# Kernel tuning notes

Measured on AMD Instinct MI355X. Metric: run time of the kernel, lower is better.

The kernel has to match this reference:

```python
import jax, jax.numpy as jnp
import numpy as np

N, D, H, B, E = 100000, 256, 256, 128, 128
STEPS = 5


def setup_inputs() -> dict:
    key = jax.random.key(0)
    ks = jax.random.split(key, 16)
    w = lambda i, shape: (jax.random.normal(ks[i], shape, jnp.float32) * 0.05)
    inp = {
        "x": jax.random.normal(ks[0], (N, D), jnp.float32),
        "batch_idxs": jnp.sort(jax.random.randint(ks[1], (N,), 0, B)),
        # FNN: Linear(D,H) -> ELU -> Linear(H,H)
        "fnn_W1": w(2, (D, H)), "fnn_b1": jnp.zeros((H,), jnp.float32),
        "fnn_W2": w(3, (H, H)), "fnn_b2": jnp.zeros((H,), jnp.float32),
        # 3-layer LSTM, input 2H (layer 0) / H (layers 1,2), hidden H
        "Wih0": w(4, (4 * H, 2 * H)), "Whh0": w(5, (4 * H, H)),
        "bih0": jnp.zeros((4 * H,), jnp.float32), "bhh0": jnp.zeros((4 * H,), jnp.float32),
        "Wih1": w(6, (4 * H, H)), "Whh1": w(7, (4 * H, H)),
        "bih1": jnp.zeros((4 * H,), jnp.float32), "bhh1": jnp.zeros((4 * H,), jnp.float32),
        "Wih2": w(8, (4 * H, H)), "Whh2": w(9, (4 * H, H)),
        "bih2": jnp.zeros((4 * H,), jnp.float32), "bhh2": jnp.zeros((4 * H,), jnp.float32),
        # output Linear(2H, E)
        "out_W": w(10, (2 * H, E)), "out_b": jnp.zeros((E,), jnp.float32),
    }
    return inp


def _lstm_cell(xin, h, c, Wih, Whh, bih, bhh):
    gates = xin @ Wih.T + bih + h @ Whh.T + bhh  # (B, 4H)
    i, f, g, o = jnp.split(gates, 4, axis=-1)    # PyTorch gate order i,f,g,o
    c = jax.nn.sigmoid(f) * c + jax.nn.sigmoid(i) * jnp.tanh(g)
    h = jax.nn.sigmoid(o) * jnp.tanh(c)
    return h, c


def reference(x, batch_idxs, fnn_W1, fnn_b1, fnn_W2, fnn_b2,
              Wih0, Whh0, bih0, bhh0, Wih1, Whh1, bih1, bhh1,
              Wih2, Whh2, bih2, bhh2, out_W, out_b):
    # FNN (ELU between layers)
    hfeat = jax.nn.elu(x @ fnn_W1 + fnn_b1) @ fnn_W2 + fnn_b2  # (N, H)

    Wihs, Whhs = (Wih0, Wih1, Wih2), (Whh0, Whh1, Whh2)
    bihs, bhhs = (bih0, bih1, bih2), (bhh0, bhh1, bhh2)
    hs = [jnp.zeros((B, H), hfeat.dtype) for _ in range(3)]
    cs = [jnp.zeros((B, H), hfeat.dtype) for _ in range(3)]
    q_star = jnp.zeros((B, 2 * H), hfeat.dtype)

    for _ in range(STEPS):
        layer_in = q_star
        for l in range(3):
            hs[l], cs[l] = _lstm_cell(layer_in, hs[l], cs[l], Wihs[l], Whhs[l], bihs[l], bhhs[l])
            layer_in = hs[l]
        q = layer_in  # (B, H)
        # segment (per-graph) attention softmax over nodes
        e = jnp.sum(hfeat * q[batch_idxs], axis=-1)                     # (N,)
        m = jax.ops.segment_max(e, batch_idxs, num_segments=B)
        m = jnp.where(jnp.isfinite(m), m, 0.0)                          # guard empty segments
        ex = jnp.exp(e - m[batch_idxs])
        denom = jax.ops.segment_sum(ex, batch_idxs, num_segments=B) + 1e-16
        a = ex / denom[batch_idxs]                                      # (N,)
        r = jax.ops.segment_sum(a[:, None] * hfeat, batch_idxs, num_segments=B)  # (B, H)
        q_star = jnp.concatenate([q, r], axis=-1)                       # (B, 2H)

    return q_star @ out_W + out_b  # (B, E)
```

## Files before the change

### kernel.cpp

```cpp
#include <hip/hip_runtime.h>

#define NN 100000
#define NSTEP 5
#define LSTR 264

typedef unsigned short ushort_t;
typedef __attribute__((ext_vector_type(8))) short short8;
typedef __attribute__((ext_vector_type(4))) float floatx4;

__device__ __forceinline__ ushort_t f2bf(float f){
  union { float f; unsigned u; } v; v.f = f;
  unsigned r = v.u + 0x7fffu + ((v.u >> 16) & 1u);
  return (ushort_t)(r >> 16);
}
__device__ __forceinline__ float bf2f(ushort_t s){
  union { unsigned u; float f; } v; v.u = ((unsigned)s) << 16;
  return v.f;
}
__device__ __forceinline__ float sigf(float x){ return 1.0f/(1.0f+__expf(-x)); }

__global__ __launch_bounds__(512, 4) void fnn_fused(const float* __restrict__ x,
    const ushort_t* __restrict__ W1P, const float* __restrict__ b1,
    const ushort_t* __restrict__ W2P, const float* __restrict__ b2,
    ushort_t* __restrict__ hfeat, int M)
{
  __shared__ ushort_t buf[64 * LSTR];
  int tid = threadIdx.x;
  int w = tid >> 6, lane = tid & 63, qd = lane >> 4, r16 = lane & 15;
  int row0 = blockIdx.x * 64;
  int col0 = w * 32;

  {
    float4 xv[8];
    #pragma unroll
    for (int it = 0; it < 8; it++){
      int idx = it * 512 + tid;
      int rg = row0 + (idx >> 6); if (rg >= M) rg = M - 1;
      xv[it] = *(const float4*)(x + (size_t)rg * 256 + (idx & 63) * 4);
    }
    #pragma unroll
    for (int it = 0; it < 8; it++){
      int idx = it * 512 + tid;
      ushort4 pk = make_ushort4(f2bf(xv[it].x), f2bf(xv[it].y), f2bf(xv[it].z), f2bf(xv[it].w));
      *(ushort4*)&buf[(idx >> 6) * LSTR + (idx & 63) * 4] = pk;
    }
  }
  __syncthreads();

  floatx4 acc[4][2];

  #pragma unroll
  for (int i=0;i<4;i++)
    #pragma unroll
    for (int j=0;j<2;j++) acc[i][j] = (floatx4){0.f,0.f,0.f,0.f};

  #pragma unroll
  for (int kc = 0; kc < 8; kc++){
    short8 af[4], bfr[2];
    #pragma unroll
    for (int i=0;i<4;i++)
      af[i] = *(const short8*)&buf[(i*16 + r16) * LSTR + kc*32 + qd*8];
    #pragma unroll
    for (int j=0;j<2;j++)
      bfr[j] = *(const short8*)(W1P + (size_t)(((w*2 + j)*8 + kc)*64 + lane)*8);
    #pragma unroll
    for (int i=0;i<4;i++)
      #pragma unroll
      for (int j=0;j<2;j++)
        acc[i][j] = __builtin_amdgcn_mfma_f32_16x16x32_bf16(af[i], bfr[j], acc[i][j], 0, 0, 0);
  }
  __syncthreads();

  #pragma unroll
  for (int i=0;i<4;i++){
    #pragma unroll
    for (int j=0;j<2;j++){
      int col = col0 + j*16 + r16;
      float bb = b1[col];
      #pragma unroll
      for (int rr=0;rr<4;rr++){
        int row = i*16 + qd*4 + rr;
        float v = acc[i][j][rr] + bb;
        v = v > 0.f ? v : (__expf(v) - 1.0f);
        buf[row * LSTR + col] = f2bf(v);
      }
    }
  }
  __syncthreads();

  #pragma unroll
  for (int i=0;i<4;i++)
    #pragma unroll
    for (int j=0;j<2;j++) acc[i][j] = (floatx4){0.f,0.f,0.f,0.f};

  #pragma unroll
  for (int kc = 0; kc < 8; kc++){
    short8 af[4], bfr[2];
    #pragma unroll
    for (int i=0;i<4;i++)
      af[i] = *(const short8*)&buf[(i*16 + r16) * LSTR + kc*32 + qd*8];
    #pragma unroll
    for (int j=0;j<2;j++)
      bfr[j] = *(const short8*)(W2P + (size_t)(((w*2 + j)*8 + kc)*64 + lane)*8);
    #pragma unroll
    for (int i=0;i<4;i++)
      #pragma unroll
      for (int j=0;j<2;j++)
        acc[i][j] = __builtin_amdgcn_mfma_f32_16x16x32_bf16(af[i], bfr[j], acc[i][j], 0, 0, 0);
  }

  #pragma unroll
  for (int i=0;i<4;i++){
    #pragma unroll
    for (int j=0;j<2;j++){
      int col = col0 + j*16 + r16;
      float bb = b2[col];
      #pragma unroll
      for (int rr=0;rr<4;rr++){
        int row = row0 + i*16 + qd*4 + rr;
        if (row < M) hfeat[(size_t)row * 256 + col] = f2bf(acc[i][j][rr] + bb);
      }
    }
  }
}

__global__ __launch_bounds__(256) void lstm_layer(const ushort_t* __restrict__ A, int lda,
    const ushort_t* __restrict__ WcP, const float* __restrict__ bcp, int KC,
    float* __restrict__ c, ushort_t* __restrict__ dstA, int sA,
    ushort_t* __restrict__ dstB, int sB, float* __restrict__ qdst)
{
  __shared__ float sbuf[3][4][256];
  int tid = threadIdx.x, w = tid >> 6, lane = tid & 63, qd = lane >> 4, r16 = lane & 15;
  int m0 = (blockIdx.x & 7) * 16, nt = blockIdx.x >> 3;
  int kcq = KC >> 2;
  int kc0 = w * kcq;

  floatx4 acc[4];
  #pragma unroll
  for (int g=0; g<4; g++) acc[g] = (floatx4){0.f,0.f,0.f,0.f};

  const ushort_t* Ar = A + (size_t)(m0 + r16) * lda + qd * 8;
  for (int kc = kc0; kc < kc0 + kcq; kc++){
    short8 av = *(const short8*)(Ar + kc*32);
    #pragma unroll
    for (int g = 0; g < 4; g++){
      short8 bv = *(const short8*)(WcP + (size_t)((((g*16 + nt)*KC) + kc)*64 + lane)*8);
      acc[g] = __builtin_amdgcn_mfma_f32_16x16x32_bf16(av, bv, acc[g], 0, 0, 0);
    }
  }
  if (w){
    #pragma unroll
    for (int g=0; g<4; g++) *(floatx4*)&sbuf[w-1][g][lane*4] = acc[g];
  }
  __syncthreads();
  if (w == 0){
    #pragma unroll
    for (int g=0; g<4; g++)
      #pragma unroll
      for (int t=0; t<3; t++){
        floatx4 p = *(floatx4*)&sbuf[t][g][lane*4];
        acc[g] = acc[g] + p;
      }
    int h = nt*16 + r16;
    float bci = bcp[h], bcf = bcp[256+h], bcg = bcp[512+h], bco = bcp[768+h];
    #pragma unroll
    for (int rr=0; rr<4; rr++){
      int row = m0 + qd*4 + rr;
      float gi = acc[0][rr] + bci;
      float gf = acc[1][rr] + bcf;
      float gg = acc[2][rr] + bcg;
      float go = acc[3][rr] + bco;
      float cp = c[row*256 + h];
      float cn = sigf(gf)*cp + sigf(gi)*tanhf(gg);
      float hn = sigf(go)*tanhf(cn);
      c[row*256 + h] = cn;
      ushort_t hb = f2bf(hn);
      dstA[row*sA + h] = hb;
      dstB[row*sB + h] = hb;
      if (qdst) qdst[row*512 + h] = hn;
    }
  }
}

__global__ __launch_bounds__(256) void attn_onepass(const ushort_t* __restrict__ hfeat,
    const int* __restrict__ seg, const float* __restrict__ q_star,
    float* __restrict__ r_part, float* __restrict__ z_part)
{
  __shared__ float sred[4][260];
  int b = blockIdx.x >> 3, p = blockIdx.x & 7;
  int w = threadIdx.x >> 6, lane = threadIdx.x & 63;
  int s0 = seg[b], s1 = seg[b+1];
  int len = s1 - s0;
  int q0 = s0 + ((len * p) >> 3);
  int q1 = s0 + ((len * (p+1)) >> 3);

  float S0=0.f, S1=0.f, S2=0.f, S3=0.f, Z=0.f;

  int n = q0 + w;
  if (n < q1){
    float4 q = *(const float4*)(q_star + (size_t)b*512 + lane*4);
    #define LOADH(nn) (*(const ushort4*)(hfeat + (size_t)(nn)*256 + lane*4))
    ushort4 ha = LOADH(n);
    ushort4 hb = ha;
    if (n + 4 < q1) hb = LOADH(n + 4);
    for (; n < q1; n += 8){
      ushort4 hc = ha, hd = hb;
      if (n + 8  < q1) hc = LOADH(n + 8);
      if (n + 12 < q1) hd = LOADH(n + 12);
      float a0=bf2f(ha.x), a1=bf2f(ha.y), a2=bf2f(ha.z), a3=bf2f(ha.w);
      float da = a0*q.x + a1*q.y + a2*q.z + a3*q.w;
      float b0=0.f,b1=0.f,b2=0.f,b3=0.f, db=0.f;
      int vB = (n + 4) < q1;
      if (vB){
        b0=bf2f(hb.x); b1=bf2f(hb.y); b2=bf2f(hb.z); b3=bf2f(hb.w);
        db = b0*q.x + b1*q.y + b2*q.z + b3*q.w;
      }
      #pragma unroll
      for (int off = 32; off; off >>= 1){
        da += __shfl_xor(da, off);
        db += __shfl_xor(db, off);
      }
      float wa = __expf(da);
      Z += wa; S0 += wa*a0; S1 += wa*a1; S2 += wa*a2; S3 += wa*a3;
      if (vB){
        float wb = __expf(db);
        Z += wb; S0 += wb*b0; S1 += wb*b1; S2 += wb*b2; S3 += wb*b3;
      }
      ha = hc; hb = hd;
    }
    #undef LOADH
  }

  *(float4*)&sred[w][lane*4] = (float4){S0, S1, S2, S3};
  if (lane == 0) sred[w][256] = Z;
  __syncthreads();
  int f = threadIdx.x;
  if (f < 256){
    float v = sred[0][f] + sred[1][f] + sred[2][f] + sred[3][f];
    r_part[((size_t)p*128 + b)*256 + f] = v;
    if (f == 0)
      z_part[p*128 + b] = sred[0][256] + sred[1][256] + sred[2][256] + sred[3][256];
  }
}

__global__ __launch_bounds__(256) void attn_fin(const float* __restrict__ r_part,
    const float* __restrict__ z_part, float* __restrict__ q_star, ushort_t* __restrict__ xc0,
    const float* __restrict__ outW, const float* __restrict__ outb,
    float* __restrict__ out, int last)
{
  __shared__ float qs[512];
  int b = blockIdx.x, f = threadIdx.x;
  float s = 0.f, z = 0.f;
  #pragma unroll
  for (int t = 0; t < 8; t++){
    s += r_part[((size_t)(t*128 + b))*256 + f];
    z += z_part[t*128 + b];
  }
  float v = s / (z + 1e-16f);
  q_star[b*512 + 256 + f] = v;
  xc0[b*768 + 256 + f] = f2bf(v);
  if (last){
    qs[f] = q_star[b*512 + f];
    qs[256 + f] = v;
    __syncthreads();
    if (f < 128){
      float acc = outb[f];
      for (int k = 0; k < 512; k++) acc += qs[k] * outW[k*128 + f];
      out[b*128 + f] = acc;
    }
  }
}

__global__ void prep_all(const float* __restrict__ W1, const float* __restrict__ W2,
    const float* __restrict__ Wih0, const float* __restrict__ Whh0,
    const float* __restrict__ Wih1, const float* __restrict__ Whh1,
    const float* __restrict__ Wih2, const float* __restrict__ Whh2,
    const float* __restrict__ bih0, const float* __restrict__ bhh0,
    const float* __restrict__ bih1, const float* __restrict__ bhh1,
    const float* __restrict__ bih2, const float* __restrict__ bhh2,
    const int* __restrict__ bidx,
    ushort_t* __restrict__ W1P, ushort_t* __restrict__ W2P,
    ushort_t* __restrict__ Wc0P, ushort_t* __restrict__ Wc1P, ushort_t* __restrict__ Wc2P,
    float* __restrict__ c, ushort_t* __restrict__ xc, float* __restrict__ q_star,
    float* __restrict__ bc, int* __restrict__ seg)
{
  int i = blockIdx.x*256 + threadIdx.x;
  if (i < 131072){
    const float* W = (i < 65536) ? W1 : W2;
    ushort_t* P = (i < 65536) ? W1P : W2P;
    int r = i & 65535;
    int T = r >> 12, r2 = r & 4095;
    int kc = r2 >> 9, l = (r2 >> 3) & 63, j = r2 & 7;
    int k = kc*32 + ((l>>4)<<3) + j;
    int n = T*16 + (l & 15);
    P[r] = f2bf(W[k*256 + n]);
    return;
  }
  i -= 131072;
  if (i < 786432){
    int T = i / 12288, r2 = i - T*12288;
    int kc = r2 >> 9, l = (r2 >> 3) & 63, j = r2 & 7;
    int k = kc*32 + ((l>>4)<<3) + j;
    int g = T >> 4, n = (T & 15)*16 + (l & 15);
    int row = g*256 + n;
    Wc0P[i] = f2bf(k < 512 ? Wih0[row*512 + k] : Whh0[row*256 + (k - 512)]);
    return;
  }
  i -= 786432;
  if (i < 1048576){
    const float* Wih = (i < 524288) ? Wih1 : Wih2;
    const float* Whh = (i < 524288) ? Whh1 : Whh2;
    ushort_t* P = (i < 524288) ? Wc1P : Wc2P;
    int r = i & 524287;
    int T = r >> 13, r2 = r & 8191;
    int kc = r2 >> 9, l = (r2 >> 3) & 63, j = r2 & 7;
    int k = kc*32 + ((l>>4)<<3) + j;
    int g = T >> 4, n = (T & 15)*16 + (l & 15);
    int row = g*256 + n;
    P[r] = f2bf(k < 256 ? Wih[row*256 + k] : Whh[row*256 + (k - 256)]);
    return;
  }
  i -= 1048576;
  if (i < 98304) { c[i] = 0.f; return; }
  i -= 98304;
  if (i < 229376) { xc[i] = 0; return; }
  i -= 229376;
  if (i < 65536) { q_star[i] = 0.f; return; }
  i -= 65536;
  if (i < 3072) {
    int l = i >> 10, g = i & 1023;
    const float* bi = (l == 0) ? bih0 : ((l == 1) ? bih1 : bih2);
    const float* bh = (l == 0) ? bhh0 : ((l == 1) ? bhh1 : bhh2);
    bc[i] = bi[g] + bh[g];
    return;
  }
  i -= 3072;
  if (i < 129) {
    int lo = 0, hi = NN;
    while (lo < hi){ int mid = (lo + hi) >> 1; if (bidx[mid] < i) lo = mid + 1; else hi = mid; }
    seg[i] = lo;
    return;
  }
}

extern "C" void kernel_launch(void* const* d_in, const int* in_sizes, int n_in,
                              void* d_out, int out_size, void* d_ws, size_t ws_size,
                              hipStream_t stream)
{
  const float* x    = (const float*)d_in[0];
  const int*   bidx = (const int*)  d_in[1];
  const float* W1   = (const float*)d_in[2];
  const float* b1   = (const float*)d_in[3];
  const float* W2   = (const float*)d_in[4];
  const float* b2   = (const float*)d_in[5];
  const float* Wih0 = (const float*)d_in[6];
  const float* Whh0 = (const float*)d_in[7];
  const float* bih0 = (const float*)d_in[8];
  const float* bhh0 = (const float*)d_in[9];
  const float* Wih1 = (const float*)d_in[10];
  const float* Whh1 = (const float*)d_in[11];
  const float* bih1 = (const float*)d_in[12];
  const float* bhh1 = (const float*)d_in[13];
  const float* Wih2 = (const float*)d_in[14];
  const float* Whh2 = (const float*)d_in[15];
  const float* bih2 = (const float*)d_in[16];
  const float* bhh2 = (const float*)d_in[17];
  const float* outW = (const float*)d_in[18];
  const float* outb = (const float*)d_in[19];

  char* p = (char*)d_ws;
  auto alloc = [&](size_t bytes)->char*{ char* r = p; p += (bytes + 255) & ~(size_t)255; return r; };
  ushort_t* hfeat  = (ushort_t*)alloc((size_t)NN*256*2);
  ushort_t* W1P    = (ushort_t*)alloc(65536*2);
  ushort_t* W2P    = (ushort_t*)alloc(65536*2);
  ushort_t* Wc0P   = (ushort_t*)alloc(786432*2);
  ushort_t* Wc1P   = (ushort_t*)alloc(524288*2);
  ushort_t* Wc2P   = (ushort_t*)alloc(524288*2);
  float*    bc     = (float*)   alloc(3072*4);
  float*    c_all  = (float*)   alloc(98304*4);
  ushort_t* xc     = (ushort_t*)alloc(229376*2);
  float*    q_star = (float*)   alloc(65536*4);
  float*    r_part = (float*)   alloc(8*128*256*4);
  float*    z_part = (float*)   alloc(8*128*4);
  int*      seg    = (int*)     alloc(129*4);

  ushort_t* xc0 = xc;
  ushort_t* xc1 = xc + 98304;
  ushort_t* xc2 = xc + 163840;
  float* c0 = c_all, *c1 = c_all + 32768, *c2 = c_all + 65536;
  float* bc0 = bc, *bc1 = bc + 1024, *bc2 = bc + 2048;

  prep_all<<<9229, 256, 0, stream>>>(W1, W2, Wih0, Whh0, Wih1, Whh1, Wih2, Whh2,
                                     bih0, bhh0, bih1, bhh1, bih2, bhh2, bidx,
                                     W1P, W2P, Wc0P, Wc1P, Wc2P,
                                     c_all, xc, q_star, bc, seg);

  fnn_fused<<<1563, 512, 0, stream>>>(x, W1P, b1, W2P, b2, hfeat, NN);

  for (int s = 0; s < NSTEP; s++){
    lstm_layer<<<128, 256, 0, stream>>>(xc0, 768, Wc0P, bc0, 24, c0, xc0 + 512, 768, xc1, 512, nullptr);
    lstm_layer<<<128, 256, 0, stream>>>(xc1, 512, Wc1P, bc1, 16, c1, xc1 + 256, 512, xc2, 512, nullptr);
    lstm_layer<<<128, 256, 0, stream>>>(xc2, 512, Wc2P, bc2, 16, c2, xc2 + 256, 512, xc0, 768, q_star);
    attn_onepass<<<1024, 256, 0, stream>>>(hfeat, seg, q_star, r_part, z_part);
    attn_fin<<<128, 256, 0, stream>>>(r_part, z_part, q_star, xc0, outW, outb,
                                      (float*)d_out, s == NSTEP-1 ? 1 : 0);
  }
}
```

Baseline: 414.6 us.

## Fuse attention finalize into next LSTM layer, pipeline FNN loads, unroll attention

The per-step attn_fin reduction now happens inside the first LSTM layer of the next step, which reads the partial sums from a transposed r_part layout and stages the result in shared memory. This removes one kernel launch per step, and a single final kernel produces the output. The FNN GEMM loops are double-buffered so LDS and weight loads overlap the MFMAs, and the occupancy hint is dropped. The attention loop processes four nodes per wave per iteration with deeper prefetch. The LSTM kernel is templated on KC so its K loop can be fully unrolled, at the cost of redundant finalize work in each of the 16 column blocks that share a row group.

```diff
diff --git a/kernel.cpp b/kernel.cpp
--- a/kernel.cpp
+++ b/kernel.cpp
@@ -19,7 +19,7 @@
 }
 __device__ __forceinline__ float sigf(float x){ return 1.0f/(1.0f+__expf(-x)); }
 
-__global__ __launch_bounds__(512, 4) void fnn_fused(const float* __restrict__ x,
+__global__ __launch_bounds__(512) void fnn_fused(const float* __restrict__ x,
     const ushort_t* __restrict__ W1P, const float* __restrict__ b1,
     const ushort_t* __restrict__ W2P, const float* __restrict__ b2,
     ushort_t* __restrict__ hfeat, int M)
@@ -30,6 +30,25 @@
   int row0 = blockIdx.x * 64;
   int col0 = w * 32;
 
+  floatx4 acc[4][2];
+  short8 afA[4], afB[4], bfA[2], bfB[2];
+
+  auto LDA = [&](short8* d, int kc){
+    #pragma unroll
+    for (int i=0;i<4;i++) d[i] = *(const short8*)&buf[(i*16 + r16)*LSTR + kc*32 + qd*8];
+  };
+  auto LDW = [&](short8* d, const ushort_t* P, int kc){
+    #pragma unroll
+    for (int j=0;j<2;j++) d[j] = *(const short8*)(P + (size_t)(((w*2 + j)*8 + kc)*64 + lane)*8);
+  };
+  auto MM = [&](short8* a, short8* b){
+    #pragma unroll
+    for (int i=0;i<4;i++)
+      #pragma unroll
+      for (int j=0;j<2;j++)
+        acc[i][j] = __builtin_amdgcn_mfma_f32_16x16x32_bf16(a[i], b[j], acc[i][j], 0, 0, 0);
+  };
+
   {
     float4 xv[8];
     #pragma unroll
@@ -45,32 +64,24 @@
       *(ushort4*)&buf[(idx >> 6) * LSTR + (idx & 63) * 4] = pk;
     }
   }
-  __syncthreads();
-
-  floatx4 acc[4][2];
+  LDW(bfA, W1P, 0);
+  __syncthreads();
 
   #pragma unroll
   for (int i=0;i<4;i++)
     #pragma unroll
     for (int j=0;j<2;j++) acc[i][j] = (floatx4){0.f,0.f,0.f,0.f};
-
-  #pragma unroll
-  for (int kc = 0; kc < 8; kc++){
-    short8 af[4], bfr[2];
-    #pragma unroll
-    for (int i=0;i<4;i++)
-      af[i] = *(const short8*)&buf[(i*16 + r16) * LSTR + kc*32 + qd*8];
-    #pragma unroll
-    for (int j=0;j<2;j++)
-      bfr[j] = *(const short8*)(W1P + (size_t)(((w*2 + j)*8 + kc)*64 + lane)*8);
-    #pragma unroll
-    for (int i=0;i<4;i++)
-      #pragma unroll
-      for (int j=0;j<2;j++)
-        acc[i][j] = __builtin_amdgcn_mfma_f32_16x16x32_bf16(af[i], bfr[j], acc[i][j], 0, 0, 0);
-  }
-  __syncthreads();
-
+  LDA(afA, 0);
+  #pragma unroll
+  for (int kc = 0; kc < 8; kc += 2){
+    if (kc + 1 < 8){ LDA(afB, kc+1); LDW(bfB, W1P, kc+1); }
+    MM(afA, bfA);
+    if (kc + 2 < 8){ LDA(afA, kc+2); LDW(bfA, W1P, kc+2); }
+    if (kc + 1 < 8) MM(afB, bfB);
+  }
+  __syncthreads();
+
+  LDW(bfA, W2P, 0);
   #pragma unroll
   for (int i=0;i<4;i++){
     #pragma unroll
@@ -92,21 +103,13 @@
   for (int i=0;i<4;i++)
     #pragma unroll
     for (int j=0;j<2;j++) acc[i][j] = (floatx4){0.f,0.f,0.f,0.f};
-
-  #pragma unroll
-  for (int kc = 0; kc < 8; kc++){
-    short8 af[4], bfr[2];
-    #pragma unroll
-    for (int i=0;i<4;i++)
-      af[i] = *(const short8*)&buf[(i*16 + r16) * LSTR + kc*32 + qd*8];
-    #pragma unroll
-    for (int j=0;j<2;j++)
-      bfr[j] = *(const short8*)(W2P + (size_t)(((w*2 + j)*8 + kc)*64 + lane)*8);
-    #pragma unroll
-    for (int i=0;i<4;i++)
-      #pragma unroll
-      for (int j=0;j<2;j++)
-        acc[i][j] = __builtin_amdgcn_mfma_f32_16x16x32_bf16(af[i], bfr[j], acc[i][j], 0, 0, 0);
+  LDA(afA, 0);
+  #pragma unroll
+  for (int kc = 0; kc < 8; kc += 2){
+    if (kc + 1 < 8){ LDA(afB, kc+1); LDW(bfB, W2P, kc+1); }
+    MM(afA, bfA);
+    if (kc + 2 < 8){ LDA(afA, kc+2); LDW(bfA, W2P, kc+2); }
+    if (kc + 1 < 8) MM(afB, bfB);
   }
 
   #pragma unroll
@@ -124,24 +127,52 @@
   }
 }
 
-__global__ __launch_bounds__(256) void lstm_layer(const ushort_t* __restrict__ A, int lda,
-    const ushort_t* __restrict__ WcP, const float* __restrict__ bcp, int KC,
+template<int KC, bool FIN>
+__global__ __launch_bounds__(256, 1) void lstm_layer(const ushort_t* __restrict__ A,
+    const ushort_t* __restrict__ WcP, const float* __restrict__ bcp,
     float* __restrict__ c, ushort_t* __restrict__ dstA, int sA,
-    ushort_t* __restrict__ dstB, int sB, float* __restrict__ qdst)
+    ushort_t* __restrict__ dstB, int sB, float* __restrict__ qdst,
+    const float* __restrict__ r_part, const float* __restrict__ z_part)
 {
   __shared__ float sbuf[3][4][256];
+  __shared__ ushort_t shr[16][264];
+  constexpr int lda = KC * 32;
+  constexpr int kcq = KC >> 2;
   int tid = threadIdx.x, w = tid >> 6, lane = tid & 63, qd = lane >> 4, r16 = lane & 15;
   int m0 = (blockIdx.x & 7) * 16, nt = blockIdx.x >> 3;
-  int kcq = KC >> 2;
+
+  if (FIN){
+    int col = tid;
+    #pragma unroll 4
+    for (int r = 0; r < 16; r++){
+      int bb = m0 + r;
+      const float* rp = r_part + ((size_t)bb*256 + col)*8;
+      float4 aa = *(const float4*)rp;
+      float4 ab = *(const float4*)(rp + 4);
+      float s = aa.x+aa.y+aa.z+aa.w + ab.x+ab.y+ab.z+ab.w;
+      const float* zp = z_part + bb*8;
+      float4 za = *(const float4*)zp;
+      float4 zb = *(const float4*)(zp + 4);
+      float z = za.x+za.y+za.z+za.w + zb.x+zb.y+zb.z+zb.w;
+      shr[r][col] = f2bf(s / (z + 1e-16f));
+    }
+    __syncthreads();
+  }
+
   int kc0 = w * kcq;
-
   floatx4 acc[4];
   #pragma unroll
   for (int g=0; g<4; g++) acc[g] = (floatx4){0.f,0.f,0.f,0.f};
 
   const ushort_t* Ar = A + (size_t)(m0 + r16) * lda + qd * 8;
-  for (int kc = kc0; kc < kc0 + kcq; kc++){
-    short8 av = *(const short8*)(Ar + kc*32);
+  #pragma unroll
+  for (int kk = 0; kk < kcq; kk++){
+    int kc = kc0 + kk;
+    short8 av;
+    if (FIN && kc >= 8 && kc < 16)
+      av = *(const short8*)&shr[r16][(kc - 8)*32 + qd*8];
+    else
+      av = *(const short8*)(Ar + kc*32);
     #pragma unroll
     for (int g = 0; g < 4; g++){
       short8 bv = *(const short8*)(WcP + (size_t)((((g*16 + nt)*KC) + kc)*64 + lane)*8);
@@ -189,46 +220,51 @@
   __shared__ float sred[4][260];
   int b = blockIdx.x >> 3, p = blockIdx.x & 7;
   int w = threadIdx.x >> 6, lane = threadIdx.x & 63;
-  int s0 = seg[b], s1 = seg[b+1];
-  int len = s1 - s0;
+  int s0 = seg[b], s1 = seg[b+1], len = s1 - s0;
   int q0 = s0 + ((len * p) >> 3);
   int q1 = s0 + ((len * (p+1)) >> 3);
 
   float S0=0.f, S1=0.f, S2=0.f, S3=0.f, Z=0.f;
-
-  int n = q0 + w;
-  if (n < q1){
-    float4 q = *(const float4*)(q_star + (size_t)b*512 + lane*4);
-    #define LOADH(nn) (*(const ushort4*)(hfeat + (size_t)(nn)*256 + lane*4))
-    ushort4 ha = LOADH(n);
-    ushort4 hb = ha;
-    if (n + 4 < q1) hb = LOADH(n + 4);
-    for (; n < q1; n += 8){
-      ushort4 hc = ha, hd = hb;
-      if (n + 8  < q1) hc = LOADH(n + 8);
-      if (n + 12 < q1) hd = LOADH(n + 12);
-      float a0=bf2f(ha.x), a1=bf2f(ha.y), a2=bf2f(ha.z), a3=bf2f(ha.w);
-      float da = a0*q.x + a1*q.y + a2*q.z + a3*q.w;
-      float b0=0.f,b1=0.f,b2=0.f,b3=0.f, db=0.f;
-      int vB = (n + 4) < q1;
-      if (vB){
-        b0=bf2f(hb.x); b1=bf2f(hb.y); b2=bf2f(hb.z); b3=bf2f(hb.w);
-        db = b0*q.x + b1*q.y + b2*q.z + b3*q.w;
+  float4 q = *(const float4*)(q_star + (size_t)b*512 + lane*4);
+
+  ushort4 cur[4];
+  int base = q0 + w;
+  #pragma unroll
+  for (int u=0;u<4;u++){
+    int n = base + 4*u;
+    cur[u] = (n < q1) ? *(const ushort4*)(hfeat + (size_t)n*256 + lane*4)
+                      : make_ushort4(0,0,0,0);
+  }
+  for (; base < q1; base += 16){
+    ushort4 nxt[4];
+    #pragma unroll
+    for (int u=0;u<4;u++){
+      int n = base + 16 + 4*u;
+      nxt[u] = (n < q1) ? *(const ushort4*)(hfeat + (size_t)n*256 + lane*4) : cur[u];
+    }
+    float fv[4][4], d[4];
+    #pragma unroll
+    for (int u=0;u<4;u++){
+      fv[u][0]=bf2f(cur[u].x); fv[u][1]=bf2f(cur[u].y);
+      fv[u][2]=bf2f(cur[u].z); fv[u][3]=bf2f(cur[u].w);
+      d[u] = fv[u][0]*q.x + fv[u][1]*q.y + fv[u][2]*q.z + fv[u][3]*q.w;
+    }
+    #pragma unroll
+    for (int off = 32; off; off >>= 1){
+      #pragma unroll
+      for (int u=0;u<4;u++) d[u] += __shfl_xor(d[u], off);
+    }
+    #pragma unroll
+    for (int u=0;u<4;u++){
+      if (base + 4*u < q1){
+        float wt = __expf(d[u]);
+        Z += wt;
+        S0 += wt*fv[u][0]; S1 += wt*fv[u][1];
+        S2 += wt*fv[u][2]; S3 += wt*fv[u][3];
       }
-      #pragma unroll
-      for (int off = 32; off; off >>= 1){
-        da += __shfl_xor(da, off);
-        db += __shfl_xor(db, off);
-      }
-      float wa = __expf(da);
-      Z += wa; S0 += wa*a0; S1 += wa*a1; S2 += wa*a2; S3 += wa*a3;
-      if (vB){
-        float wb = __expf(db);
-        Z += wb; S0 += wb*b0; S1 += wb*b1; S2 += wb*b2; S3 += wb*b3;
-      }
-      ha = hc; hb = hd;
-    }
-    #undef LOADH
+    }
+    #pragma unroll
+    for (int u=0;u<4;u++) cur[u] = nxt[u];
   }
 
   *(float4*)&sred[w][lane*4] = (float4){S0, S1, S2, S3};
@@ -237,37 +273,34 @@
   int f = threadIdx.x;
   if (f < 256){
     float v = sred[0][f] + sred[1][f] + sred[2][f] + sred[3][f];
-    r_part[((size_t)p*128 + b)*256 + f] = v;
+    r_part[((size_t)b*256 + f)*8 + p] = v;
     if (f == 0)
-      z_part[p*128 + b] = sred[0][256] + sred[1][256] + sred[2][256] + sred[3][256];
+      z_part[b*8 + p] = sred[0][256] + sred[1][256] + sred[2][256] + sred[3][256];
   }
 }
 
 __global__ __launch_bounds__(256) void attn_fin(const float* __restrict__ r_part,
-    const float* __restrict__ z_part, float* __restrict__ q_star, ushort_t* __restrict__ xc0,
+    const float* __restrict__ z_part, const float* __restrict__ q_star,
     const float* __restrict__ outW, const float* __restrict__ outb,
-    float* __restrict__ out, int last)
+    float* __restrict__ out)
 {
   __shared__ float qs[512];
   int b = blockIdx.x, f = threadIdx.x;
-  float s = 0.f, z = 0.f;
-  #pragma unroll
-  for (int t = 0; t < 8; t++){
-    s += r_part[((size_t)(t*128 + b))*256 + f];
-    z += z_part[t*128 + b];
-  }
-  float v = s / (z + 1e-16f);
-  q_star[b*512 + 256 + f] = v;
-  xc0[b*768 + 256 + f] = f2bf(v);
-  if (last){
-    qs[f] = q_star[b*512 + f];
-    qs[256 + f] = v;
-    __syncthreads();
-    if (f < 128){
-      float acc = outb[f];
-      for (int k = 0; k < 512; k++) acc += qs[k] * outW[k*128 + f];
-      out[b*128 + f] = acc;
-    }
+  const float* rp = r_part + ((size_t)b*256 + f)*8;
+  float4 aa = *(const float4*)rp;
+  float4 ab = *(const float4*)(rp + 4);
+  float s = aa.x+aa.y+aa.z+aa.w + ab.x+ab.y+ab.z+ab.w;
+  const float* zp = z_part + b*8;
+  float4 za = *(const float4*)zp;
+  float4 zb = *(const float4*)(zp + 4);
+  float z = za.x+za.y+za.z+za.w + zb.x+zb.y+zb.z+zb.w;
+  qs[256 + f] = s / (z + 1e-16f);
+  qs[f] = q_star[b*512 + f];
+  __syncthreads();
+  if (f < 128){
+    float acc = outb[f];
+    for (int k = 0; k < 512; k++) acc += qs[k] * outW[k*128 + f];
+    out[b*128 + f] = acc;
   }
 }
 
@@ -380,8 +413,8 @@
   float*    c_all  = (float*)   alloc(98304*4);
   ushort_t* xc     = (ushort_t*)alloc(229376*2);
   float*    q_star = (float*)   alloc(65536*4);
-  float*    r_part = (float*)   alloc(8*128*256*4);
-  float*    z_part = (float*)   alloc(8*128*4);
+  float*    r_part = (float*)   alloc((size_t)128*256*8*4);
+  float*    z_part = (float*)   alloc(128*8*4);
   int*      seg    = (int*)     alloc(129*4);
 
   ushort_t* xc0 = xc;
@@ -398,11 +431,17 @@
   fnn_fused<<<1563, 512, 0, stream>>>(x, W1P, b1, W2P, b2, hfeat, NN);
 
   for (int s = 0; s < NSTEP; s++){
-    lstm_layer<<<128, 256, 0, stream>>>(xc0, 768, Wc0P, bc0, 24, c0, xc0 + 512, 768, xc1, 512, nullptr);
-    lstm_layer<<<128, 256, 0, stream>>>(xc1, 512, Wc1P, bc1, 16, c1, xc1 + 256, 512, xc2, 512, nullptr);
-    lstm_layer<<<128, 256, 0, stream>>>(xc2, 512, Wc2P, bc2, 16, c2, xc2 + 256, 512, xc0, 768, q_star);
+    if (s == 0)
+      lstm_layer<24,false><<<128, 256, 0, stream>>>(xc0, Wc0P, bc0, c0,
+          xc0 + 512, 768, xc1, 512, nullptr, nullptr, nullptr);
+    else
+      lstm_layer<24,true><<<128, 256, 0, stream>>>(xc0, Wc0P, bc0, c0,
+          xc0 + 512, 768, xc1, 512, nullptr, r_part, z_part);
+    lstm_layer<16,false><<<128, 256, 0, stream>>>(xc1, Wc1P, bc1, c1,
+        xc1 + 256, 512, xc2, 512, nullptr, nullptr, nullptr);
+    lstm_layer<16,false><<<128, 256, 0, stream>>>(xc2, Wc2P, bc2, c2,
+        xc2 + 256, 512, xc0, 768, q_star, nullptr, nullptr);
     attn_onepass<<<1024, 256, 0, stream>>>(hfeat, seg, q_star, r_part, z_part);
-    attn_fin<<<128, 256, 0, stream>>>(r_part, z_part, q_star, xc0, outW, outb,
-                                      (float*)d_out, s == NSTEP-1 ? 1 : 0);
-  }
-}
+  }
+  attn_fin<<<128, 256, 0, stream>>>(r_part, z_part, q_star, outW, outb, (float*)d_out);
+}
```

Result: slower. 448.1 us (+8.1%).
